# Kernel tuning notes

Hardware: AMD Instinct MI355X
Metric: run time of the kernel (lower is better)

The kernel has to match this reference:

```python
import jax, jax.numpy as jnp
import numpy as np

N, T0, T1 = 2, 4, 8
H, W = 128, 128
PD, AD = 4, 4
Z_POS, Z_APP = PD * PD, AD * AD
Z = Z_POS + Z_APP
KS, STRIDE, ROUTINGS = 3, 1, 3


def psquash(p, axis):
    return p / jnp.max(jnp.abs(p), axis=axis, keepdims=True)


def matwo_squash(p, axis):
    sq = jnp.sum(p * p, axis=axis, keepdims=True)
    return sq / (1.0 + sq) * p / jnp.sqrt(sq + 1e-9)


def setup_inputs() -> dict:
    key = jax.random.key(0)
    ks = jax.random.split(key, 5)
    return {
        "x": jax.random.normal(ks[0], (N, T0, Z, H, W), jnp.float32),
        "W_conv": jax.random.normal(ks[1], (T0, KS, KS, 1, T1), jnp.float32) * 0.1,
        "W_pos": jax.random.normal(ks[2], (T0, Z_POS, T1), jnp.float32) * 0.1,
        "W_app": jax.random.normal(ks[3], (T0, Z_APP, T1), jnp.float32) * 0.1,
        "b_app": jax.random.normal(ks[4], (T0, T1), jnp.float32) * 0.1,
    }


def _forward(x, W_conv, W_pos, W_app, b_app):
    n, t0, z0, h, w = x.shape
    t1 = W_conv.shape[-1]
    # per-input-capsule 2D conv: channels folded into batch, 1 -> t1 channels
    xt = x.transpose(1, 0, 2, 3, 4).reshape(t0, n * z0, h, w, 1)
    conv = jax.vmap(lambda u, k: jax.lax.conv_general_dilated(
        u, k, (STRIDE, STRIDE), 'SAME',
        dimension_numbers=('NHWC', 'HWIO', 'NHWC')))(xt, W_conv)
    h1, w1 = conv.shape[2], conv.shape[3]
    # [t0, N, z0, H1, W1, t1] -> [t0, N, H1, W1, t1, z0] -> flatten (t1,z0)
    u = conv.reshape(t0, n, z0, h1, w1, t1).transpose(0, 1, 3, 4, 5, 2)
    flat = u.reshape(t0, n, h1, w1, t1 * z0)
    # faithful replication of the original tf.split on the flattened (t1*z0) axis
    u_pos = flat[..., :t1 * Z_POS].reshape(t0, n, h1, w1, t1, PD, PD)
    u_app = flat[..., t1 * Z_POS:].reshape(t0, n, h1, w1, t1, AD, AD)

    # pose transform matrices: l2-normalize columns (axis=-2), coordinate addition
    mult_pos = W_pos.reshape(t0, t1, PD, PD)
    mult_pos = mult_pos / jnp.sqrt(
        jnp.maximum(jnp.sum(mult_pos * mult_pos, axis=-2, keepdims=True), 1e-12))
    coord = jnp.zeros((h1, w1, 1, PD, PD), x.dtype)
    coord = coord.at[:, :, 0, -1, 0].add(jnp.arange(w1, dtype=x.dtype)[None, :] / w1)
    coord = coord.at[:, :, 0, -1, 1].add(jnp.arange(h1, dtype=x.dtype)[:, None] / h1)
    mult_pos_hw = mult_pos[:, None, None] + coord[None]  # [t0,h1,w1,t1,PD,PD]
    u_hat_pos = jnp.einsum('cnhwtij,chwtjk->cnhwtik', u_pos, mult_pos_hw)

    mult_app = W_app.reshape(t0, t1, AD, AD)
    u_app = u_app + b_app[:, None, None, None, :, None, None]
    u_hat_app = jnp.einsum('cnhwtij,ctjk->cnhwtik', u_app, mult_app)

    u_hat = jnp.concatenate(
        [u_hat_pos.reshape(t0, n, h1, w1, t1, Z_POS),
         u_hat_app.reshape(t0, n, h1, w1, t1, Z_APP)], axis=-1)
    u_hat = u_hat.transpose(1, 5, 2, 3, 0, 4)  # [N, z1, H1, W1, t0, t1]

    # dual routing (sigmoid coupling, separate pos/app agreement)
    uh_pos, uh_app = u_hat[:, :Z_POS], u_hat[:, Z_POS:]
    b = jnp.zeros((n, h1, w1, t0, t1), x.dtype)
    for _ in range(ROUTINGS - 1):
        r = jax.nn.sigmoid(b)
        p = jnp.einsum('nzhwct,nhwct->nzhwt', u_hat, r)
        v_pos = psquash(p[:, :Z_POS], axis=1)
        v_app = matwo_squash(p[:, Z_POS:], axis=1)
        rout = (jnp.einsum('nzhwct,nzhwt->nhwct', uh_pos, v_pos)
                * jnp.einsum('nzhwct,nzhwt->nhwct', uh_app, v_app))
        b = b + rout
    c = jax.nn.sigmoid(b)
    p = jnp.einsum('nzhwct,nhwct->nzhwt', u_hat, c)
    v = jnp.concatenate([psquash(p[:, :Z_POS], axis=1),
                         matwo_squash(p[:, Z_POS:], axis=1)], axis=1)
    return v.transpose(0, 4, 1, 2, 3)  # [N, t1, z1, H1, W1]


def reference(x, W_conv, W_pos, W_app, b_app):
    return _forward(x, W_conv, W_pos, W_app, b_app)
```

## Files before the change

kernel.cpp:

```cpp
#include <hip/hip_runtime.h>
#include <cmath>


#define TH 4
#define TW 8
#define XR (TH + 2)
#define XC (TW + 2)
#define ZPAD 36

__global__ __launch_bounds__(256, 3)
void caps_fused(const float* __restrict__ x,
                const float* __restrict__ Wc,
                const float* __restrict__ Wp,
                const float* __restrict__ Wa,
                const float* __restrict__ ba,
                float* __restrict__ out)
{
    __shared__ float xs[XR][XC][4][ZPAD];

    const int tid = threadIdx.x;
    const int n  = blockIdx.z;
    const int h0 = blockIdx.y * TH;
    const int w0 = blockIdx.x * TW;

    for (int e = tid; e < 128 * XR * XC; e += 256) {
        int col = e % XC;
        int tmp = e / XC;
        int row = tmp % XR;
        int cz  = tmp / XR;
        int gh = h0 - 1 + row;
        int gw = w0 - 1 + col;
        float v = 0.0f;
        if ((unsigned)gh < 128u && (unsigned)gw < 128u)
            v = x[(((size_t)(n * 128 + cz)) << 14) + (gh << 7) + gw];
        xs[row][col][cz >> 5][cz & 31] = v;
    }

    const int p    = tid >> 5;
    const int lane = tid & 31;
    const int c    = lane & 3;
    const int t    = lane >> 2;
    const int chp  = t >> 1;
    const int zoff = (t & 1) << 4;

    float wp9[9], wa9[9];
#pragma unroll
    for (int i = 0; i < 9; ++i) {
        wp9[i] = Wc[(c * 9 + i) * 8 + chp];
        wa9[i] = Wc[(c * 9 + i) * 8 + 4 + chp];
    }
    float Mp[16], Ma[16];
#pragma unroll
    for (int q = 0; q < 16; ++q) {
        Mp[q] = Wp[c * 128 + t * 16 + q];
        Ma[q] = Wa[c * 128 + t * 16 + q];
    }
#pragma unroll
    for (int k = 0; k < 4; ++k) {
        float s = Mp[k] * Mp[k] + Mp[4 + k] * Mp[4 + k]
                + Mp[8 + k] * Mp[8 + k] + Mp[12 + k] * Mp[12 + k];
        float inv = 1.0f / sqrtf(fmaxf(s, 1e-12f));
        Mp[k] *= inv; Mp[4 + k] *= inv; Mp[8 + k] *= inv; Mp[12 + k] *= inv;
    }
    const float bap = ba[c * 8 + t];
    const float wx  = (float)(w0 + p) * (1.0f / 128.0f);

    __syncthreads();

    for (int g = 0; g < TH; ++g) {
        float up[16], ua[16];
#pragma unroll
        for (int q = 0; q < 16; ++q) { up[q] = 0.0f; ua[q] = 0.0f; }
#pragma unroll
        for (int dy = 0; dy < 3; ++dy) {
#pragma unroll
            for (int dx = 0; dx < 3; ++dx) {
                const float* bp = &xs[g + dy][p + dx][c][zoff];
                float xv[16];
                *(float4*)&xv[0]  = *(const float4*)(bp);
                *(float4*)&xv[4]  = *(const float4*)(bp + 4);
                *(float4*)&xv[8]  = *(const float4*)(bp + 8);
                *(float4*)&xv[12] = *(const float4*)(bp + 12);
                const float w1 = wp9[dy * 3 + dx];
                const float w2 = wa9[dy * 3 + dx];
#pragma unroll
                for (int q = 0; q < 16; ++q) {
                    up[q] += xv[q] * w1;
                    ua[q] += xv[q] * w2;
                }
            }
        }

        const float hy = (float)(h0 + g) * (1.0f / 128.0f);
        float uh[32];
#pragma unroll
        for (int i = 0; i < 4; ++i) {
#pragma unroll
            for (int k = 0; k < 4; ++k) {
                uh[i * 4 + k] = up[i * 4 + 0] * Mp[k]
                              + up[i * 4 + 1] * Mp[4 + k]
                              + up[i * 4 + 2] * Mp[8 + k]
                              + up[i * 4 + 3] * Mp[12 + k];
            }
            uh[i * 4 + 0] += up[i * 4 + 3] * wx;
            uh[i * 4 + 1] += up[i * 4 + 3] * hy;
        }
#pragma unroll
        for (int i = 0; i < 4; ++i) {
            const float a0 = ua[i * 4 + 0] + bap;
            const float a1 = ua[i * 4 + 1] + bap;
            const float a2 = ua[i * 4 + 2] + bap;
            const float a3 = ua[i * 4 + 3] + bap;
#pragma unroll
            for (int k = 0; k < 4; ++k)
                uh[16 + i * 4 + k] = a0 * Ma[k] + a1 * Ma[4 + k]
                                   + a2 * Ma[8 + k] + a3 * Ma[12 + k];
        }

        float bacc = 0.0f;
#pragma unroll
        for (int it = 0; it < 3; ++it) {
            const float r = 1.0f / (1.0f + expf(-bacc));
            float pz[32];
#pragma unroll
            for (int zz = 0; zz < 32; ++zz) {
                float v = uh[zz] * r;
                v += __shfl_xor(v, 1, 64);
                v += __shfl_xor(v, 2, 64);
                pz[zz] = v;
            }
            float mx = 0.0f;
#pragma unroll
            for (int zz = 0; zz < 16; ++zz) mx = fmaxf(mx, fabsf(pz[zz]));
            const float invm = 1.0f / mx;
            float sq = 0.0f;
#pragma unroll
            for (int zz = 16; zz < 32; ++zz) sq += pz[zz] * pz[zz];
            const float fac = sq / ((1.0f + sq) * sqrtf(sq + 1e-9f));

            if (it < 2) {
                float dp = 0.0f, da = 0.0f;
#pragma unroll
                for (int zz = 0; zz < 16; ++zz) dp += uh[zz] * pz[zz];
#pragma unroll
                for (int zz = 16; zz < 32; ++zz) da += uh[zz] * pz[zz];
                bacc += (dp * invm) * (da * fac);
            } else if (c == 0) {
                const int row = h0 + g;
                float* ob = out + (((size_t)((n * 8 + t) * 32)) << 14)
                                + (row << 7) + (w0 + p);
#pragma unroll
                for (int zz = 0; zz < 16; ++zz)
                    ob[((size_t)zz) << 14] = pz[zz] * invm;
#pragma unroll
                for (int zz = 16; zz < 32; ++zz)
                    ob[((size_t)zz) << 14] = pz[zz] * fac;
            }
        }
    }
}

extern "C" void kernel_launch(void* const* d_in, const int* in_sizes, int n_in,
                              void* d_out, int out_size, void* d_ws, size_t ws_size,
                              hipStream_t stream) {
    const float* x  = (const float*)d_in[0];
    const float* Wc = (const float*)d_in[1];
    const float* Wp = (const float*)d_in[2];
    const float* Wa = (const float*)d_in[3];
    const float* ba = (const float*)d_in[4];
    float* out = (float*)d_out;

    dim3 grid(128 / TW, 128 / TH, 2);
    caps_fused<<<grid, 256, 0, stream>>>(x, Wc, Wp, Wa, ba, out);
}
```

Before: 142.2 us.

## Halve tile height, swizzle shared layout, use DPP quad reductions and fast exp

```diff
diff --git a/kernel.cpp b/kernel.cpp
--- a/kernel.cpp
+++ b/kernel.cpp
@@ -2,13 +2,21 @@
 #include <cmath>
 
 
-#define TH 4
+#define TH 2
 #define TW 8
 #define XR (TH + 2)
 #define XC (TW + 2)
 #define ZPAD 36
 
-__global__ __launch_bounds__(256, 3)
+__device__ __forceinline__ float qsum4(float v) {
+    int a = __builtin_amdgcn_mov_dpp(__float_as_int(v), 0xB1, 0xF, 0xF, true);
+    v += __int_as_float(a);
+    int b = __builtin_amdgcn_mov_dpp(__float_as_int(v), 0x4E, 0xF, 0xF, true);
+    v += __int_as_float(b);
+    return v;
+}
+
+__global__ __launch_bounds__(256, 4)
 void caps_fused(const float* __restrict__ x,
                 const float* __restrict__ Wc,
                 const float* __restrict__ Wp,
@@ -33,7 +41,9 @@
         float v = 0.0f;
         if ((unsigned)gh < 128u && (unsigned)gw < 128u)
             v = x[(((size_t)(n * 128 + cz)) << 14) + (gh << 7) + gw];
-        xs[row][col][cz >> 5][cz & 31] = v;
+        int z = cz & 31;
+        int s = (row * XC + col) & 7;
+        xs[row][col][cz >> 5][((((z >> 2) & 7) ^ s) << 2) | (z & 3)] = v;
     }
 
     const int p    = tid >> 5;
@@ -41,7 +51,7 @@
     const int c    = lane & 3;
     const int t    = lane >> 2;
     const int chp  = t >> 1;
-    const int zoff = (t & 1) << 4;
+    const int q0   = (t & 1) << 2;
 
     float wp9[9], wa9[9];
 #pragma unroll
@@ -75,12 +85,14 @@
         for (int dy = 0; dy < 3; ++dy) {
 #pragma unroll
             for (int dx = 0; dx < 3; ++dx) {
-                const float* bp = &xs[g + dy][p + dx][c][zoff];
+                const int rr = g + dy, cc = p + dx;
+                const int s = (rr * XC + cc) & 7;
+                const float* bp = &xs[rr][cc][c][0];
                 float xv[16];
-                *(float4*)&xv[0]  = *(const float4*)(bp);
-                *(float4*)&xv[4]  = *(const float4*)(bp + 4);
-                *(float4*)&xv[8]  = *(const float4*)(bp + 8);
-                *(float4*)&xv[12] = *(const float4*)(bp + 12);
+                *(float4*)&xv[0]  = *(const float4*)(bp + (((q0 | 0) ^ s) << 2));
+                *(float4*)&xv[4]  = *(const float4*)(bp + (((q0 | 1) ^ s) << 2));
+                *(float4*)&xv[8]  = *(const float4*)(bp + (((q0 | 2) ^ s) << 2));
+                *(float4*)&xv[12] = *(const float4*)(bp + (((q0 | 3) ^ s) << 2));
                 const float w1 = wp9[dy * 3 + dx];
                 const float w2 = wa9[dy * 3 + dx];
 #pragma unroll
@@ -120,15 +132,12 @@
         float bacc = 0.0f;
 #pragma unroll
         for (int it = 0; it < 3; ++it) {
-            const float r = 1.0f / (1.0f + expf(-bacc));
+            const float r = 1.0f / (1.0f + __expf(-bacc));
             float pz[32];
 #pragma unroll
-            for (int zz = 0; zz < 32; ++zz) {
-                float v = uh[zz] * r;
-                v += __shfl_xor(v, 1, 64);
-                v += __shfl_xor(v, 2, 64);
-                pz[zz] = v;
-            }
+            for (int zz = 0; zz < 32; ++zz)
+                pz[zz] = qsum4(uh[zz] * r);
+
             float mx = 0.0f;
 #pragma unroll
             for (int zz = 0; zz < 16; ++zz) mx = fmaxf(mx, fabsf(pz[zz]));
```

Result: faster. 139.4 us (-2.0%).
